# Kernel tuning notes

Hardware: AMD Instinct MI355X
Metric: run time of the kernel (lower is better)

The kernel has to match this reference:

```python
import jax, jax.numpy as jnp
import numpy as np

B, H, W = 2, 64, 64
D = 256  # in_channels
EPS = 1e-5


def conv2d(x, w, pad):
    # x: NCHW, w: OIHW
    return jax.lax.conv_general_dilated(
        x, w, window_strides=(1, 1), padding=[(pad, pad), (pad, pad)],
        dimension_numbers=("NCHW", "OIHW", "NCHW"))


def code_projection(X, codewords, scale):
    # X: [B, D, H, W]; codewords: [K, D]; scale: [D, K]
    b, d = X.shape[0], X.shape[1]
    x = X.reshape(b, d, -1).transpose(0, 2, 1)              # [B, N, D]
    # residual: [B, N, D, K] (large broadcast tensor, as in the original)
    residual = (x[:, :, :, None] - codewords.T[None, None]) * scale
    Q = jax.nn.softmax(-0.5 * jnp.sum(residual ** 2, axis=2), axis=-1)  # [B, N, K]
    Z_num = jnp.einsum("bnk,bndk->bdk", Q, residual)        # sum over N
    Z_ = Z_num / Q.sum(axis=1)[:, None, :]                  # [B, D, K]
    Z = Z_ / jnp.sqrt(jnp.sum(Z_ ** 2, axis=1, keepdims=True))  # L2 over D
    return Z, Q


def graph_conv(inp, weight, gamma, beta):
    # inp: [B, D, K]
    adj = jnp.einsum("bdk,bdl->bkl", inp, inp)              # input^T @ input
    support = jnp.einsum("ij,bjk->bik", weight, inp)        # weight @ input
    out = jnp.einsum("bdk,bkl->bdl", support, adj)          # support @ adj
    out = jax.nn.relu(out)
    # BatchNorm1d (training-mode batch stats over (B, K) per channel D)
    mean = out.mean(axis=(0, 2), keepdims=True)
    var = out.var(axis=(0, 2), keepdims=True)
    return gamma[None, :, None] * (out - mean) / jnp.sqrt(var + EPS) + beta[None, :, None]


def reproj(graph, Q, h, w):
    # graph: [B, D, K], Q: [B, N, K]
    x = jnp.einsum("bdk,bnk->bdn", graph, Q)
    return x.reshape(graph.shape[0], graph.shape[1], h, w)


def branch(c, conv_w, cw, sc, gcnw, g, bta, ext_w, h, w):
    z, q = code_projection(conv2d(c, conv_w, 1), cw, sc)
    z = graph_conv(z, gcnw, g, bta)
    return conv2d(reproj(z, q, h, w), ext_w, 0) + c


def setup_inputs() -> dict:
    key = jax.random.key(0)
    keys = iter(jax.random.split(key, 64))
    nk = lambda: next(keys)
    inp = {}
    inp["c3"] = jax.random.normal(nk(), (B, 512, H, W), jnp.float32)
    inp["c4"] = jax.random.normal(nk(), (B, 512, H, W), jnp.float32)
    inp["c5"] = jax.random.normal(nk(), (B, 512, H, W), jnp.float32)
    for name, K in [("32", 32), ("16", 16), ("8", 8)]:
        inp[f"conv{name}_w"] = jax.random.normal(nk(), (256, 512, 3, 3), jnp.float32) * 0.02
        std1 = 1.0 / np.sqrt(K * D)
        inp[f"cw{name}"] = jax.random.uniform(nk(), (K, D), jnp.float32, -std1, std1)
        inp[f"sc{name}"] = jax.random.uniform(nk(), (D, K), jnp.float32, -1.0, 0.0)
        stdv = 1.0 / np.sqrt(D)
        inp[f"gcnw{name}"] = jax.random.uniform(nk(), (D, D), jnp.float32, -stdv, stdv)
        inp[f"bng{name}"] = jax.random.uniform(nk(), (D,), jnp.float32, 0.5, 1.5)
        inp[f"bnb{name}"] = jax.random.normal(nk(), (D,), jnp.float32) * 0.1
        inp[f"ext{name}_w"] = jax.random.normal(nk(), (512, 256, 1, 1), jnp.float32) * 0.05
    inp["smooth_w"] = jax.random.normal(nk(), (512, 1536, 3, 3), jnp.float32) * 0.01
    inp["smg"] = jax.random.uniform(nk(), (512,), jnp.float32, 0.5, 1.5)
    inp["smb"] = jax.random.normal(nk(), (512,), jnp.float32) * 0.1
    return inp


def reference(c3, c4, c5,
              conv32_w, cw32, sc32, gcnw32, bng32, bnb32, ext32_w,
              conv16_w, cw16, sc16, gcnw16, bng16, bnb16, ext16_w,
              conv8_w, cw8, sc8, gcnw8, bng8, bnb8, ext8_w,
              smooth_w, smg, smb):
    h, w = c3.shape[2], c3.shape[3]
    x_32 = branch(c3, conv32_w, cw32, sc32, gcnw32, bng32, bnb32, ext32_w, h, w)
    x_16 = branch(c4, conv16_w, cw16, sc16, gcnw16, bng16, bnb16, ext16_w, h, w)
    x_8 = branch(c5, conv8_w, cw8, sc8, gcnw8, bng8, bnb8, ext8_w, h, w)
    out = jnp.concatenate([x_8, x_16, x_32], axis=1)        # [B, 1536, H, W]
    out = conv2d(out, smooth_w, 1)
    # BatchNorm2d (training-mode batch stats) + ReLU
    mean = out.mean(axis=(0, 2, 3), keepdims=True)
    var = out.var(axis=(0, 2, 3), keepdims=True)
    out = smg[None, :, None, None] * (out - mean) / jnp.sqrt(var + EPS) + smb[None, :, None, None]
    return jax.nn.relu(out)
```

## Files before the change

### kernel.cpp

```cpp
#include <hip/hip_runtime.h>
#include <hip/hip_bf16.h>
#include <math.h>

#define HWN 4096
#define DCH 256
#define EPSV 1e-5f

typedef unsigned short u16;
typedef __attribute__((ext_vector_type(8))) short short8b;
typedef __attribute__((ext_vector_type(4))) float fx4;
typedef __attribute__((ext_vector_type(8))) unsigned short u16x8;

static __device__ inline u16 f2bf(float f) {
  __hip_bfloat16 h = __float2bfloat16(f);
  return *reinterpret_cast<u16*>(&h);
}
static __device__ inline float bf2f(u16 u) {
  unsigned int v = ((unsigned int)u) << 16;
  return __uint_as_float(v);
}

__global__ __launch_bounds__(256) void t_chwc3_k(const float* __restrict__ i0p,
    const float* __restrict__ i1p, const float* __restrict__ i2p,
    u16* __restrict__ out) {
  __shared__ float tl[32][257];
  const int p0 = blockIdx.x * 256, cic = blockIdx.y;
  const int z = blockIdx.z;
  const int br = z >> 1, b = z & 1;
  const float* in = (br == 0) ? i0p : ((br == 1) ? i1p : i2p);
  const int t = threadIdx.x;
  const float* ip = in + ((size_t)(b * 512 + cic * 32)) * HWN + p0;
#pragma unroll
  for (int r = 0; r < 32; ++r) tl[r][t] = ip[(size_t)r * HWN + t];
  __syncthreads();
  u16* op = out + ((size_t)((z * 16 + cic)) * HWN + p0 + t) * 32;
#pragma unroll
  for (int g = 0; g < 4; ++g) {
    u16x8 o;
#pragma unroll
    for (int j = 0; j < 8; ++j) o[j] = f2bf(tl[g * 8 + j][t]);
    *reinterpret_cast<u16x8*>(op + g * 8) = o;
  }
}

template<int CIN, int COUT>
__global__ __launch_bounds__(256) void wpack_k(const float* __restrict__ w0,
    const float* __restrict__ w1, const float* __restrict__ w2,
    u16* __restrict__ wp) {
  constexpr int NCIC = CIN / 32, NCOG = COUT / 16;
  const int br = blockIdx.y;
  const float* w = (br == 0) ? w0 : ((br == 1) ? w1 : w2);
  u16* wpb = wp + (size_t)br * 9 * NCIC * NCOG * 512;
  const int cog = blockIdx.x % NCOG, cic = blockIdx.x / NCOG;
  __shared__ float ws_[16 * 32 * 9];
  const int t = threadIdx.x;
  const float* src = w + ((size_t)(cog * 16) * CIN + cic * 32) * 9;
  for (int i = t; i < 4608; i += 256) {
    int co = i / 288, r = i % 288;
    ws_[i] = src[(size_t)co * CIN * 9 + r];
  }
  __syncthreads();
  const size_t tapstride = (size_t)NCIC * NCOG * 512;
  const size_t base = ((size_t)cic * NCOG + cog) * 512;
#pragma unroll
  for (int tap = 0; tap < 9; ++tap) {
#pragma unroll
    for (int e0 = 0; e0 < 512; e0 += 256) {
      int e = e0 + t;
      int kg = e >> 7, m = (e >> 3) & 15, j = e & 7;
      wpb[tap * tapstride + base + e] = f2bf(ws_[m * 288 + (kg * 8 + j) * 9 + tap]);
    }
  }
}

template<int CIN, int COUT, int SPLIT, int COW, int WPE, bool BF16OUT>
__global__ __launch_bounds__(256, WPE) void convsp_k(
    const u16* __restrict__ xt, const u16* __restrict__ wp,
    void* __restrict__ outv) {
  constexpr int NCIC = CIN / 32;
  constexpr int NCO = COUT / COW;
  constexpr int NWT = COW / 16;
  constexpr int CICPS = NCIC / SPLIT;
  constexpr size_t OUTEL = (size_t)2 * COUT * HWN;
  const int br = blockIdx.y;
  xt += (size_t)br * 2 * NCIC * HWN * 32;
  wp += (size_t)br * 9 * NCIC * (COUT / 16) * 512;

  int g = blockIdx.x;
  const int cpx = (int)gridDim.x >> 3;
  g = (g & 7) * cpx + (g >> 3);
  const int s = g / (32 * NCO);
  const int rem = g % (32 * NCO);
  const int rt = rem / NCO;
  const int cob = (rem % NCO) * COW;

  const int wv = threadIdx.x >> 6, lane = threadIdx.x & 63;
  const int row = rt * 4 + wv;
  const int b = row >> 6, h = row & 63;
  const int m = lane & 15, kg = lane >> 4;

  fx4 acc[4][NWT];
#pragma unroll
  for (int i = 0; i < 4; ++i)
#pragma unroll
    for (int jn = 0; jn < NWT; ++jn) acc[i][jn] = (fx4){0.f, 0.f, 0.f, 0.f};

  const short8b zero8 = (short8b){0, 0, 0, 0, 0, 0, 0, 0};

#pragma unroll 1
  for (int cic = s * CICPS; cic < (s + 1) * CICPS; ++cic) {
    const u16* xbase = xt + ((size_t)(b * NCIC + cic)) * HWN * 32;
#pragma unroll
    for (int ty = 0; ty < 3; ++ty) {
      const int hh = h + ty - 1;
      if ((unsigned)hh < 64u) {
        const u16* rowp = xbase + (size_t)hh * 2048 + kg * 8;
#pragma unroll
        for (int tx = 0; tx < 3; ++tx) {
          short8b a[4];
#pragma unroll
          for (int mt = 0; mt < 4; ++mt) {
            int wi = mt * 16 + m + tx - 1;
            bool ok = ((unsigned)wi < 64u);
            int wc = ok ? wi : 0;
            short8b v = *reinterpret_cast<const short8b*>(rowp + wc * 32);
            a[mt] = ok ? v : zero8;
          }
          const int tap = ty * 3 + tx;
          const u16* wt = wp + (((size_t)tap * NCIC + cic) * (COUT / 16)
                                + (cob >> 4)) * 512 + lane * 8;
          short8b bb[NWT];
#pragma unroll
          for (int nt = 0; nt < NWT; ++nt)
            bb[nt] = *reinterpret_cast<const short8b*>(wt + nt * 512);
#pragma unroll
          for (int mt = 0; mt < 4; ++mt)
#pragma unroll
            for (int nt = 0; nt < NWT; ++nt)
              acc[mt][nt] = __builtin_amdgcn_mfma_f32_16x16x32_bf16(a[mt], bb[nt], acc[mt][nt], 0, 0, 0);
        }
      }
    }
  }

#pragma unroll
  for (int mt = 0; mt < 4; ++mt)
#pragma unroll
    for (int nt = 0; nt < NWT; ++nt) {
      int co = cob + nt * 16 + m;
      size_t idx = ((size_t)(b * COUT + co)) * HWN + h * 64 + mt * 16 + kg * 4;
      if (BF16OUT) {
        u16* op = (u16*)outv + (size_t)(br * SPLIT + s) * OUTEL + idx;
        ushort4 o;
        o.x = f2bf(acc[mt][nt][0]); o.y = f2bf(acc[mt][nt][1]);
        o.z = f2bf(acc[mt][nt][2]); o.w = f2bf(acc[mt][nt][3]);
        *reinterpret_cast<ushort4*>(op) = o;
      } else {
        float* op = (float*)outv + (size_t)(br * SPLIT + s) * OUTEL + idx;
        *reinterpret_cast<fx4*>(op) = acc[mt][nt];
      }
    }
}

__global__ __launch_bounds__(256) void breduce_k(const u16* __restrict__ slab,
    float* __restrict__ X) {
  const int br = blockIdx.x >> 10;
  const size_t el = (size_t)2 * DCH * HWN;
  const u16* sb = slab + (size_t)br * 2 * el;
  float* Xb = X + (size_t)br * el;
  const size_t i0 = ((size_t)(blockIdx.x & 1023) * 256 + threadIdx.x) * 8;
  u16x8 s0 = *reinterpret_cast<const u16x8*>(sb + i0);
  u16x8 s1 = *reinterpret_cast<const u16x8*>(sb + el + i0);
  fx4 o0, o1;
#pragma unroll
  for (int j = 0; j < 4; ++j) o0[j] = bf2f(s0[j]) + bf2f(s1[j]);
#pragma unroll
  for (int j = 0; j < 4; ++j) o1[j] = bf2f(s0[4 + j]) + bf2f(s1[4 + j]);
  *reinterpret_cast<fx4*>(Xb + i0) = o0;
  *reinterpret_cast<fx4*>(Xb + i0 + 4) = o1;
}

__global__ __launch_bounds__(256) void sreduce_bn_k(const u16* __restrict__ slab,
    float* __restrict__ dout, float* __restrict__ pstat) {
  const int o = blockIdx.x, b = blockIdx.y;
  const size_t el = (size_t)2 * 512 * HWN;
  const size_t base = ((size_t)(b * 512 + o)) * HWN;
  const int t = threadIdx.x;
  float s = 0.f, ss = 0.f;
#pragma unroll
  for (int i0 = t * 8; i0 < HWN; i0 += 256 * 8) {
    u16x8 v0 = *reinterpret_cast<const u16x8*>(slab + base + i0);
    u16x8 v1 = *reinterpret_cast<const u16x8*>(slab + el + base + i0);
    u16x8 v2 = *reinterpret_cast<const u16x8*>(slab + 2 * el + base + i0);
    u16x8 v3 = *reinterpret_cast<const u16x8*>(slab + 3 * el + base + i0);
    fx4 y0, y1;
#pragma unroll
    for (int j = 0; j < 4; ++j) {
      float y = (bf2f(v0[j]) + bf2f(v1[j])) + (bf2f(v2[j]) + bf2f(v3[j]));
      y0[j] = y; s += y; ss = fmaf(y, y, ss);
    }
#pragma unroll
    for (int j = 0; j < 4; ++j) {
      float y = (bf2f(v0[4 + j]) + bf2f(v1[4 + j])) + (bf2f(v2[4 + j]) + bf2f(v3[4 + j]));
      y1[j] = y; s += y; ss = fmaf(y, y, ss);
    }
    *reinterpret_cast<fx4*>(dout + base + i0) = y0;
    *reinterpret_cast<fx4*>(dout + base + i0 + 4) = y1;
  }
  __shared__ float rs[4], rss[4];
  for (int off = 32; off; off >>= 1) { s += __shfl_down(s, off); ss += __shfl_down(ss, off); }
  int lane = t & 63, wid = t >> 6;
  if (lane == 0) { rs[wid] = s; rss[wid] = ss; }
  __syncthreads();
  if (t == 0) {
    pstat[(b * 512 + o) * 2]     = rs[0] + rs[1] + rs[2] + rs[3];
    pstat[(b * 512 + o) * 2 + 1] = rss[0] + rss[1] + rss[2] + rss[3];
  }
}

__global__ __launch_bounds__(512) void bnfin_k(const float* __restrict__ pstat,
    float* __restrict__ stat) {
  const int o = threadIdx.x;
  float S  = pstat[o * 2] + pstat[(512 + o) * 2];
  float SS = pstat[o * 2 + 1] + pstat[(512 + o) * 2 + 1];
  float mean = S / (2 * HWN);
  float var  = SS / (2 * HWN) - mean * mean;
  stat[o] = mean;
  stat[512 + o] = 1.f / sqrtf(var + EPSV);
}

__global__ __launch_bounds__(256) void prep3_k(
    const float* __restrict__ sc0, const float* __restrict__ sc1, const float* __restrict__ sc2,
    const float* __restrict__ cw0, const float* __restrict__ cw1, const float* __restrict__ cw2,
    float2* __restrict__ AB, float* __restrict__ Ck) {
  const int br = blockIdx.y;
  const int K = 8 << br;
  const int k = blockIdx.x;
  if (k >= K) return;
  const float* sc = (br == 0) ? sc0 : ((br == 1) ? sc1 : sc2);
  const float* cw = (br == 0) ? cw0 : ((br == 1) ? cw1 : cw2);
  float2* ABb = AB + 2048 * ((1 << br) - 1);
  float* Ckb = Ck + 8 * ((1 << br) - 1);
  const int d = threadIdx.x;
  float s = sc[d * K + k];
  float a = s * s;
  float c = cw[k * DCH + d];
  ABb[d * K + k] = make_float2(a, c * a);
  float tt = c * s;
  tt = tt * tt;
  __shared__ float red[4];
  for (int off = 32; off; off >>= 1) tt += __shfl_down(tt, off);
  int lane = threadIdx.x & 63, wid = threadIdx.x >> 6;
  if (lane == 0) red[wid] = tt;
  __syncthreads();
  if (threadIdx.x == 0) Ckb[k] = red[0] + red[1] + red[2] + red[3];
}

template<int K>
static __device__ void score_body(int b, float* sm, const float* __restrict__ X,
    const float2* __restrict__ AB, const float* __restrict__ Ck,
    float* __restrict__ Qt, float* __restrict__ Qsp) {
  const int lane = threadIdx.x & 63;
  const int g = threadIdx.x >> 6;
  const int n = blockIdx.x * 64 + lane;
  const float* xp = X + ((size_t)b * DCH) * HWN + n;
  float s_[K];
#pragma unroll
  for (int k = 0; k < K; ++k) s_[k] = 0.f;
  for (int d = g * 64; d < g * 64 + 64; ++d) {
    float xv = xp[(size_t)d * HWN];
    float x2 = xv * xv;
    float xm = -2.f * xv;
    const float2* abp = AB + d * K;
#pragma unroll
    for (int k = 0; k < K; ++k) {
      float2 ab = abp[k];
      s_[k] = fmaf(x2, ab.x, s_[k]);
      s_[k] = fmaf(xm, ab.y, s_[k]);
    }
  }
  float* smr = sm + (g * 64 + lane) * (K + 1);
#pragma unroll
  for (int k = 0; k < K; ++k) smr[k] = s_[k];
  __syncthreads();
  if (g == 0) {
    const float* r0 = sm + lane * (K + 1);
    const float* r1 = sm + (64 + lane) * (K + 1);
    const float* r2 = sm + (128 + lane) * (K + 1);
    const float* r3 = sm + (192 + lane) * (K + 1);
    float mx = -1e30f;
#pragma unroll
    for (int k = 0; k < K; ++k) {
      float v = (r0[k] + r1[k]) + (r2[k] + r3[k]);
      s_[k] = -0.5f * (v + Ck[k]);
      mx = fmaxf(mx, s_[k]);
    }
    float sum = 0.f;
#pragma unroll
    for (int k = 0; k < K; ++k) { float e = expf(s_[k] - mx); s_[k] = e; sum += e; }
    float inv = 1.f / sum;
#pragma unroll
    for (int k = 0; k < K; ++k) {
      float v = s_[k] * inv;
      Qt[((size_t)(b * K + k)) * HWN + n] = v;
      for (int off = 32; off; off >>= 1) v += __shfl_down(v, off);
      if (lane == 0) Qsp[((size_t)(b * K + k)) * 64 + blockIdx.x] = v;
    }
  }
}

__global__ __launch_bounds__(256) void score3_k(const float* __restrict__ X3,
    const float2* __restrict__ AB3, const float* __restrict__ Ck3,
    float* __restrict__ Qt3, float* __restrict__ Qsp3) {
  __shared__ float sm[4 * 64 * 33];
  const int z = blockIdx.y, br = z >> 1, b = z & 1;
  const size_t XEL = (size_t)2 * DCH * HWN;
  if (br == 0)
    score_body<8>(b, sm, X3, AB3, Ck3, Qt3, Qsp3);
  else if (br == 1)
    score_body<16>(b, sm, X3 + XEL, AB3 + 2048, Ck3 + 8, Qt3 + 65536, Qsp3 + 1024);
  else
    score_body<32>(b, sm, X3 + 2 * XEL, AB3 + 6144, Ck3 + 24, Qt3 + 196608, Qsp3 + 3072);
}

template<int K>
static __device__ void mmulp_body(int b, float* xs, float* pw,
    const float* __restrict__ X, const float* __restrict__ Qt,
    float* __restrict__ Mp) {
  const int d = blockIdx.x, nch = blockIdx.y;
  const int t = threadIdx.x;
  const float* xp = X + ((size_t)(b * DCH + d)) * HWN + nch * 512;
  xs[t] = xp[t]; xs[t + 256] = xp[t + 256];
  __syncthreads();
  const int lane = t & 63, wid = t >> 6;
#pragma unroll
  for (int k = 0; k < K; ++k) {
    const float* qp = Qt + ((size_t)(b * K + k)) * HWN + nch * 512;
    float s = fmaf(xs[t], qp[t], xs[t + 256] * qp[t + 256]);
    for (int off = 32; off; off >>= 1) s += __shfl_down(s, off);
    if (lane == 0) pw[wid * 33 + k] = s;
  }
  __syncthreads();
  if (t < K)
    Mp[(((size_t)(b * DCH + d)) * K + t) * 8 + nch] =
        (pw[t] + pw[33 + t]) + (pw[66 + t] + pw[99 + t]);
}

__global__ __launch_bounds__(256) void mmulp3_k(const float* __restrict__ X3,
    const float* __restrict__ Qt3, float* __restrict__ Mp3) {
  __shared__ float xs[512];
  __shared__ float pw[4 * 33];
  const int z = blockIdx.z, br = z >> 1, b = z & 1;
  const size_t XEL = (size_t)2 * DCH * HWN;
  if (br == 0)
    mmulp_body<8>(b, xs, pw, X3, Qt3, Mp3);
  else if (br == 1)
    mmulp_body<16>(b, xs, pw, X3 + XEL, Qt3 + 65536, Mp3 + 32768);
  else
    mmulp_body<32>(b, xs, pw, X3 + 2 * XEL, Qt3 + 196608, Mp3 + 98304);
}

template<int K>
static __device__ void fuse1_body(int b, float* buf, const float* __restrict__ Mp,
    const float* __restrict__ Qsp, const float* __restrict__ sc,
    const float* __restrict__ cw, const float* __restrict__ Wm,
    float* __restrict__ Graw) {
  float* zl = buf;
  float* adj = zl + DCH * K;
  float* rn = adj + K * K;
  float* qsl = rn + K;
  const int t = threadIdx.x;
  if (t < K) {
    const float* qp = Qsp + ((size_t)(b * K + t)) * 64;
    float s = 0.f;
    for (int i = 0; i < 64; ++i) s += qp[i];
    qsl[t] = s;
  }
  __syncthreads();
#pragma unroll
  for (int k = 0; k < K; ++k) {
    const float* mp = Mp + (((size_t)(b * DCH + t)) * K + k) * 8;
    fx4 p0 = *reinterpret_cast<const fx4*>(mp);
    fx4 p1 = *reinterpret_cast<const fx4*>(mp + 4);
    float mm = ((p0[0] + p0[1]) + (p0[2] + p0[3])) + ((p1[0] + p1[1]) + (p1[2] + p1[3]));
    float qs = qsl[k];
    zl[t * K + k] = sc[t * K + k] * (mm - cw[k * DCH + t] * qs) / qs;
  }
  __syncthreads();
  if (t < K) {
    float s = 0.f;
    for (int i = 0; i < DCH; ++i) { float v = zl[i * K + t]; s = fmaf(v, v, s); }
    rn[t] = 1.f / sqrtf(s);
  }
  __syncthreads();
#pragma unroll
  for (int k = 0; k < K; ++k) zl[t * K + k] *= rn[k];
  __syncthreads();
  for (int p = t; p < K * K; p += 256) {
    int k = p / K, l = p % K;
    float s = 0.f;
    for (int i = 0; i < DCH; ++i) s = fmaf(zl[i * K + k], zl[i * K + l], s);
    adj[p] = s;
  }
  __syncthreads();
  float sup[K];
#pragma unroll
  for (int k = 0; k < K; ++k) sup[k] = 0.f;
  const float* wr = Wm + (size_t)t * DCH;
  for (int jj = 0; jj < DCH; ++jj) {
    float wv = wr[jj];
#pragma unroll
    for (int k = 0; k < K; ++k) sup[k] = fmaf(wv, zl[jj * K + k], sup[k]);
  }
#pragma unroll
  for (int l = 0; l < K; ++l) {
    float s = 0.f;
#pragma unroll
    for (int k = 0; k < K; ++k) s = fmaf(sup[k], adj[k * K + l], s);
    Graw[((size_t)(b * DCH + t)) * K + l] = fmaxf(s, 0.f);
  }
}

__global__ __launch_bounds__(256) void fuse13_k(const float* __restrict__ Mp3,
    const float* __restrict__ Qsp3,
    const float* __restrict__ sc0, const float* __restrict__ sc1, const float* __restrict__ sc2,
    const float* __restrict__ cw0, const float* __restrict__ cw1, const float* __restrict__ cw2,
    const float* __restrict__ wm0, const float* __restrict__ wm1, const float* __restrict__ wm2,
    float* __restrict__ Graw3) {
  __shared__ float buf[DCH * 32 + 32 * 32 + 64];
  const int z = blockIdx.x, br = z >> 1, b = z & 1;
  if (br == 0)
    fuse1_body<8>(b, buf, Mp3, Qsp3, sc0, cw0, wm0, Graw3);
  else if (br == 1)
    fuse1_body<16>(b, buf, Mp3 + 32768, Qsp3 + 1024, sc1, cw1, wm1, Graw3 + 4096);
  else
    fuse1_body<32>(b, buf, Mp3 + 98304, Qsp3 + 3072, sc2, cw2, wm2, Graw3 + 12288);
}

template<int K>
static __device__ void fuse2_body(int b, int ob, float* gl,
    const float* __restrict__ Graw, const float* __restrict__ gamma,
    const float* __restrict__ beta, const float* __restrict__ E,
    float* __restrict__ EG) {
  const int t = threadIdx.x;
  {
    const int d = t;
    float s = 0.f, ss = 0.f;
#pragma unroll
    for (int b2 = 0; b2 < 2; ++b2)
#pragma unroll
      for (int l = 0; l < K; ++l) {
        float v = Graw[((size_t)(b2 * DCH + d)) * K + l];
        s += v; ss = fmaf(v, v, ss);
      }
    const float invn = 1.f / (2 * K);
    float mean = s * invn;
    float var  = ss * invn - mean * mean;
    float giv  = gamma[d] / sqrtf(var + EPSV);
    float be   = beta[d];
#pragma unroll
    for (int l = 0; l < K; ++l) {
      float v = Graw[((size_t)(b * DCH + d)) * K + l];
      gl[d * K + l] = fmaf(v - mean, giv, be);
    }
  }
  __syncthreads();
  const int o = ob * 256 + t;
  float a[K];
#pragma unroll
  for (int k = 0; k < K; ++k) a[k] = 0.f;
  const fx4* e4 = reinterpret_cast<const fx4*>(E + (size_t)o * DCH);
  for (int d4 = 0; d4 < 64; ++d4) {
    fx4 v = e4[d4];
#pragma unroll
    for (int j = 0; j < 4; ++j) {
      float vv = v[j];
#pragma unroll
      for (int k = 0; k < K; ++k)
        a[k] = fmaf(vv, gl[(d4 * 4 + j) * K + k], a[k]);
    }
  }
#pragma unroll
  for (int k = 0; k < K; ++k)
    EG[((size_t)(b * 512 + o)) * K + k] = a[k];
}

__global__ __launch_bounds__(256) void fuse23_k(const float* __restrict__ Graw3,
    const float* __restrict__ g0, const float* __restrict__ g1, const float* __restrict__ g2,
    const float* __restrict__ b0, const float* __restrict__ b1, const float* __restrict__ b2,
    const float* __restrict__ e0, const float* __restrict__ e1, const float* __restrict__ e2,
    float* __restrict__ EG3) {
  __shared__ float gl[DCH * 32];
  const int b = blockIdx.x, ob = blockIdx.y, br = blockIdx.z;
  if (br == 0)
    fuse2_body<8>(b, ob, gl, Graw3, g0, b0, e0, EG3);
  else if (br == 1)
    fuse2_body<16>(b, ob, gl, Graw3 + 4096, g1, b1, e1, EG3 + 8192);
  else
    fuse2_body<32>(b, ob, gl, Graw3 + 12288, g2, b2, e2, EG3 + 24576);
}

template<int K>
static __device__ void yout_body(int b, u16* egl, const float* __restrict__ EG,
    const float* __restrict__ Qt, const float* __restrict__ cres,
    u16* __restrict__ cat, int coff) {
  const int cg = blockIdx.y;
  const int t = threadIdx.x;
  const int lane = t & 63, sub = t >> 6;
  const int n = blockIdx.x * 64 + lane;
  for (int i = t; i < K * 128; i += 256) {
    int k = i >> 7, co = i & 127;
    egl[i] = f2bf(EG[((size_t)(b * 512 + cg * 128 + co)) * K + k]);
  }
  float q[K];
#pragma unroll
  for (int k = 0; k < K; ++k) q[k] = Qt[((size_t)(b * K + k)) * HWN + n];
  __syncthreads();
  const float* crow = cres + (size_t)b * 512 * HWN + n;
#pragma unroll
  for (int it = 0; it < 4; ++it) {
    int co = sub * 32 + it * 8;
    int gco = cg * 128 + co;
    float y[8];
#pragma unroll
    for (int jj = 0; jj < 8; ++jj) y[jj] = crow[(size_t)(gco + jj) * HWN];
#pragma unroll
    for (int k = 0; k < K; ++k) {
      u16x8 eg = *reinterpret_cast<const u16x8*>(&egl[k * 128 + co]);
#pragma unroll
      for (int jj = 0; jj < 8; ++jj) y[jj] = fmaf(bf2f(eg[jj]), q[k], y[jj]);
    }
    u16x8 o;
#pragma unroll
    for (int jj = 0; jj < 8; ++jj) o[jj] = f2bf(y[jj]);
    int ch = coff + gco;
    *reinterpret_cast<u16x8*>(cat +
        (((size_t)(b * 48 + (ch >> 5)) * HWN + n) * 32 + (ch & 31))) = o;
  }
}

__global__ __launch_bounds__(256) void yout3_k(const float* __restrict__ EG3,
    const float* __restrict__ Qt3, const float* __restrict__ c5,
    const float* __restrict__ c4, const float* __restrict__ c3,
    u16* __restrict__ cat) {
  __shared__ u16 egl[32 * 128];
  const int z = blockIdx.z, br = z >> 1, b = z & 1;
  if (br == 0)
    yout_body<8>(b, egl, EG3, Qt3, c5, cat, 0);
  else if (br == 1)
    yout_body<16>(b, egl, EG3 + 8192, Qt3 + 65536, c4, cat, 512);
  else
    yout_body<32>(b, egl, EG3 + 24576, Qt3 + 196608, c3, cat, 1024);
}

__global__ __launch_bounds__(256) void bnrelu_k(float* __restrict__ out,
    const float* __restrict__ stat, const float* __restrict__ g,
    const float* __restrict__ bb) {
  int idx = blockIdx.x * 256 + threadIdx.x;
  int o = (idx >> 12) & 511;
  float v = out[idx];
  float r = fmaf((v - stat[o]) * stat[512 + o], g[o], bb[o]);
  out[idx] = fmaxf(r, 0.f);
}

extern "C" void kernel_launch(void* const* d_in, const int* in_sizes, int n_in,
                              void* d_out, int out_size, void* d_ws, size_t ws_size,
                              hipStream_t stream) {
  const float* c3 = (const float*)d_in[0];
  const float* c4 = (const float*)d_in[1];
  const float* c5 = (const float*)d_in[2];
  const float* smooth_w = (const float*)d_in[24];
  const float* smg = (const float*)d_in[25];
  const float* smb = (const float*)d_in[26];
  float* dout = (float*)d_out;

  char* wsb = (char*)d_ws;
  u16* Xt3 = (u16*)wsb;
  u16* cat = (u16*)wsb;
  u16* Wb  = (u16*)(wsb + 25165824);
  float* stat  = (float*)(wsb + 39321600);
  float* pstat = (float*)(wsb + 39325696);
  float* pool  = (float*)(wsb + 39346176);
  char* C = wsb + 43540480;
  u16* bslab   = (u16*)C;
  float* X3    = (float*)(C + 25165824);
  u16* sslab   = (u16*)C;

  float* Qt3  = pool;
  float* Qsp3 = pool + 458752;
  float* Mp3  = pool + 465920;
  float* Graw3 = pool + 723968;
  float* EG3  = pool + 752640;
  float2* AB3 = (float2*)(pool + 809984);
  float* Ck3  = pool + 838656;

  t_chwc3_k<<<dim3(16, 16, 6), 256, 0, stream>>>(c5, c4, c3, Xt3);
  wpack_k<512, 256><<<dim3(256, 3), 256, 0, stream>>>(
      (const float*)d_in[17], (const float*)d_in[10], (const float*)d_in[3], Wb);
  convsp_k<512, 256, 2, 64, 4, true><<<dim3(256, 3), 256, 0, stream>>>(Xt3, Wb, bslab);
  breduce_k<<<3072, 256, 0, stream>>>(bslab, X3);

  prep3_k<<<dim3(32, 3), 256, 0, stream>>>(
      (const float*)d_in[19], (const float*)d_in[12], (const float*)d_in[5],
      (const float*)d_in[18], (const float*)d_in[11], (const float*)d_in[4],
      AB3, Ck3);
  score3_k<<<dim3(64, 6), 256, 0, stream>>>(X3, AB3, Ck3, Qt3, Qsp3);
  mmulp3_k<<<dim3(256, 8, 6), 256, 0, stream>>>(X3, Qt3, Mp3);
  fuse13_k<<<6, 256, 0, stream>>>(Mp3, Qsp3,
      (const float*)d_in[19], (const float*)d_in[12], (const float*)d_in[5],
      (const float*)d_in[18], (const float*)d_in[11], (const float*)d_in[4],
      (const float*)d_in[20], (const float*)d_in[13], (const float*)d_in[6],
      Graw3);
  fuse23_k<<<dim3(2, 2, 3), 256, 0, stream>>>(Graw3,
      (const float*)d_in[21], (const float*)d_in[14], (const float*)d_in[7],
      (const float*)d_in[22], (const float*)d_in[15], (const float*)d_in[8],
      (const float*)d_in[23], (const float*)d_in[16], (const float*)d_in[9],
      EG3);
  yout3_k<<<dim3(64, 4, 6), 256, 0, stream>>>(EG3, Qt3, c5, c4, c3, cat);

  wpack_k<1536, 512><<<dim3(1536, 1), 256, 0, stream>>>(smooth_w, smooth_w, smooth_w, Wb);
  convsp_k<1536, 512, 4, 128, 2, true><<<dim3(512, 1), 256, 0, stream>>>(cat, Wb, sslab);
  sreduce_bn_k<<<dim3(512, 2), 256, 0, stream>>>(sslab, dout, pstat);
  bnfin_k<<<1, 512, 0, stream>>>(pstat, stat);
  bnrelu_k<<<16384, 256, 0, stream>>>(dout, stat, smg, smb);
}
```

Measured before the change: 488.6 us.

## Stage conv weights in double-buffered LDS and fuse split-K reduce into scoring

The implicit-GEMM conv kernel now cooperatively loads each tap-row's weight tiles into a double-buffered shared-memory array, prefetching the next stage into registers while MFMAs run on the current one. Previously every wave loaded the weights straight from global memory. Separately, the standalone bf16 split-K reduction kernel is removed, and the scoring kernel sums the two partial slabs itself, writing X on the fly. This cuts global weight traffic and one kernel launch with its extra pass over the data. In exchange it adds shared-memory use, a barrier per stage, and lower occupancy (the first conv's launch bound drops from 4 to 3 waves per EU).

```diff
diff --git a/kernel.cpp b/kernel.cpp
--- a/kernel.cpp
+++ b/kernel.cpp
@@ -74,14 +74,20 @@
 }
 
 template<int CIN, int COUT, int SPLIT, int COW, int WPE, bool BF16OUT>
-__global__ __launch_bounds__(256, WPE) void convsp_k(
+__global__ __launch_bounds__(256, WPE) void convlds_k(
     const u16* __restrict__ xt, const u16* __restrict__ wp,
     void* __restrict__ outv) {
   constexpr int NCIC = CIN / 32;
   constexpr int NCO = COUT / COW;
   constexpr int NWT = COW / 16;
   constexpr int CICPS = NCIC / SPLIT;
+  constexpr int NST = CICPS * 3;
+  constexpr int TAPB = COW * 32;
+  constexpr int WSH = TAPB / 4;
+  constexpr int RNDS = WSH / 512;
   constexpr size_t OUTEL = (size_t)2 * COUT * HWN;
+  __shared__ u16 bl[2][3 * TAPB];
+
   const int br = blockIdx.y;
   xt += (size_t)br * 2 * NCIC * HWN * 32;
   wp += (size_t)br * 9 * NCIC * (COUT / 16) * 512;
@@ -98,6 +104,7 @@
   const int row = rt * 4 + wv;
   const int b = row >> 6, h = row & 63;
   const int m = lane & 15, kg = lane >> 4;
+  const int cic0 = s * CICPS;
 
   fx4 acc[4][NWT];
 #pragma unroll
@@ -106,41 +113,74 @@
     for (int jn = 0; jn < NWT; ++jn) acc[i][jn] = (fx4){0.f, 0.f, 0.f, 0.f};
 
   const short8b zero8 = (short8b){0, 0, 0, 0, 0, 0, 0, 0};
+  const int lds_lane = wv * WSH + lane * 8;
+
+  {
+    const int cic = cic0, ty = 0;
+#pragma unroll
+    for (int t3 = 0; t3 < 3; ++t3) {
+      const int tap = ty * 3 + t3;
+      const u16* srcb = wp + (((size_t)tap * NCIC + cic) * (COUT / 16) + (cob >> 4)) * 512;
+#pragma unroll
+      for (int r = 0; r < RNDS; ++r) {
+        u16x8 v = *reinterpret_cast<const u16x8*>(srcb + lds_lane + r * 512);
+        *reinterpret_cast<u16x8*>(&bl[0][t3 * TAPB + lds_lane + r * 512]) = v;
+      }
+    }
+  }
+  __syncthreads();
 
 #pragma unroll 1
-  for (int cic = s * CICPS; cic < (s + 1) * CICPS; ++cic) {
-    const u16* xbase = xt + ((size_t)(b * NCIC + cic)) * HWN * 32;
-#pragma unroll
-    for (int ty = 0; ty < 3; ++ty) {
-      const int hh = h + ty - 1;
-      if ((unsigned)hh < 64u) {
-        const u16* rowp = xbase + (size_t)hh * 2048 + kg * 8;
-#pragma unroll
-        for (int tx = 0; tx < 3; ++tx) {
-          short8b a[4];
-#pragma unroll
-          for (int mt = 0; mt < 4; ++mt) {
-            int wi = mt * 16 + m + tx - 1;
-            bool ok = ((unsigned)wi < 64u);
-            int wc = ok ? wi : 0;
-            short8b v = *reinterpret_cast<const short8b*>(rowp + wc * 32);
-            a[mt] = ok ? v : zero8;
-          }
-          const int tap = ty * 3 + tx;
-          const u16* wt = wp + (((size_t)tap * NCIC + cic) * (COUT / 16)
-                                + (cob >> 4)) * 512 + lane * 8;
-          short8b bb[NWT];
+  for (int st = 0; st < NST; ++st) {
+    const int cur = st & 1;
+    u16x8 stg[3][RNDS];
+    const bool hasnext = (st + 1 < NST);
+    if (hasnext) {
+      const int cicn = cic0 + (st + 1) / 3, tyn = (st + 1) % 3;
+#pragma unroll
+      for (int t3 = 0; t3 < 3; ++t3) {
+        const int tap = tyn * 3 + t3;
+        const u16* srcb = wp + (((size_t)tap * NCIC + cicn) * (COUT / 16) + (cob >> 4)) * 512;
+#pragma unroll
+        for (int r = 0; r < RNDS; ++r)
+          stg[t3][r] = *reinterpret_cast<const u16x8*>(srcb + lds_lane + r * 512);
+      }
+    }
+    const int cic = cic0 + st / 3, ty = st % 3;
+    const int hh = h + ty - 1;
+    if ((unsigned)hh < 64u) {
+      const u16* rowp = xt + ((size_t)(b * NCIC + cic)) * HWN * 32
+                        + (size_t)hh * 2048 + kg * 8;
+#pragma unroll
+      for (int tx = 0; tx < 3; ++tx) {
+        short8b a[4];
+#pragma unroll
+        for (int mt = 0; mt < 4; ++mt) {
+          int wi = mt * 16 + m + tx - 1;
+          bool ok = ((unsigned)wi < 64u);
+          int wc = ok ? wi : 0;
+          short8b v = *reinterpret_cast<const short8b*>(rowp + wc * 32);
+          a[mt] = ok ? v : zero8;
+        }
+        short8b bb[NWT];
+#pragma unroll
+        for (int nt = 0; nt < NWT; ++nt)
+          bb[nt] = *reinterpret_cast<const short8b*>(&bl[cur][tx * TAPB + nt * 512 + lane * 8]);
+#pragma unroll
+        for (int mt = 0; mt < 4; ++mt)
 #pragma unroll
           for (int nt = 0; nt < NWT; ++nt)
-            bb[nt] = *reinterpret_cast<const short8b*>(wt + nt * 512);
-#pragma unroll
-          for (int mt = 0; mt < 4; ++mt)
-#pragma unroll
-            for (int nt = 0; nt < NWT; ++nt)
-              acc[mt][nt] = __builtin_amdgcn_mfma_f32_16x16x32_bf16(a[mt], bb[nt], acc[mt][nt], 0, 0, 0);
-        }
+            acc[mt][nt] = __builtin_amdgcn_mfma_f32_16x16x32_bf16(a[mt], bb[nt], acc[mt][nt], 0, 0, 0);
       }
     }
+    if (hasnext) {
+#pragma unroll
+      for (int t3 = 0; t3 < 3; ++t3)
+#pragma unroll
+        for (int r = 0; r < RNDS; ++r)
+          *reinterpret_cast<u16x8*>(&bl[cur ^ 1][t3 * TAPB + lds_lane + r * 512]) = stg[t3][r];
+    }
+    __syncthreads();
   }
 
 #pragma unroll
@@ -160,24 +200,6 @@
         *reinterpret_cast<fx4*>(op) = acc[mt][nt];
       }
     }
-}
-
-__global__ __launch_bounds__(256) void breduce_k(const u16* __restrict__ slab,
-    float* __restrict__ X) {
-  const int br = blockIdx.x >> 10;
-  const size_t el = (size_t)2 * DCH * HWN;
-  const u16* sb = slab + (size_t)br * 2 * el;
-  float* Xb = X + (size_t)br * el;
-  const size_t i0 = ((size_t)(blockIdx.x & 1023) * 256 + threadIdx.x) * 8;
-  u16x8 s0 = *reinterpret_cast<const u16x8*>(sb + i0);
-  u16x8 s1 = *reinterpret_cast<const u16x8*>(sb + el + i0);
-  fx4 o0, o1;
-#pragma unroll
-  for (int j = 0; j < 4; ++j) o0[j] = bf2f(s0[j]) + bf2f(s1[j]);
-#pragma unroll
-  for (int j = 0; j < 4; ++j) o1[j] = bf2f(s0[4 + j]) + bf2f(s1[4 + j]);
-  *reinterpret_cast<fx4*>(Xb + i0) = o0;
-  *reinterpret_cast<fx4*>(Xb + i0 + 4) = o1;
 }
 
 __global__ __launch_bounds__(256) void sreduce_bn_k(const u16* __restrict__ slab,
@@ -257,18 +279,22 @@
 }
 
 template<int K>
-static __device__ void score_body(int b, float* sm, const float* __restrict__ X,
+static __device__ void score_body(int b, float* sm,
+    const u16* __restrict__ s0p, const u16* __restrict__ s1p,
+    float* __restrict__ Xout,
     const float2* __restrict__ AB, const float* __restrict__ Ck,
     float* __restrict__ Qt, float* __restrict__ Qsp) {
   const int lane = threadIdx.x & 63;
   const int g = threadIdx.x >> 6;
   const int n = blockIdx.x * 64 + lane;
-  const float* xp = X + ((size_t)b * DCH) * HWN + n;
+  const size_t bbase = ((size_t)b * DCH) * HWN + n;
   float s_[K];
 #pragma unroll
   for (int k = 0; k < K; ++k) s_[k] = 0.f;
   for (int d = g * 64; d < g * 64 + 64; ++d) {
-    float xv = xp[(size_t)d * HWN];
+    const size_t ofs = bbase + (size_t)d * HWN;
+    float xv = bf2f(s0p[ofs]) + bf2f(s1p[ofs]);
+    Xout[ofs] = xv;
     float x2 = xv * xv;
     float xm = -2.f * xv;
     const float2* abp = AB + d * K;
@@ -309,18 +335,21 @@
   }
 }
 
-__global__ __launch_bounds__(256) void score3_k(const float* __restrict__ X3,
+__global__ __launch_bounds__(256) void score3_k(const u16* __restrict__ bslab,
+    float* __restrict__ X3,
     const float2* __restrict__ AB3, const float* __restrict__ Ck3,
     float* __restrict__ Qt3, float* __restrict__ Qsp3) {
   __shared__ float sm[4 * 64 * 33];
   const int z = blockIdx.y, br = z >> 1, b = z & 1;
   const size_t XEL = (size_t)2 * DCH * HWN;
+  const u16* s0 = bslab + (size_t)br * 2 * XEL;
+  const u16* s1 = s0 + XEL;
   if (br == 0)
-    score_body<8>(b, sm, X3, AB3, Ck3, Qt3, Qsp3);
+    score_body<8>(b, sm, s0, s1, X3, AB3, Ck3, Qt3, Qsp3);
   else if (br == 1)
-    score_body<16>(b, sm, X3 + XEL, AB3 + 2048, Ck3 + 8, Qt3 + 65536, Qsp3 + 1024);
+    score_body<16>(b, sm, s0, s1, X3 + XEL, AB3 + 2048, Ck3 + 8, Qt3 + 65536, Qsp3 + 1024);
   else
-    score_body<32>(b, sm, X3 + 2 * XEL, AB3 + 6144, Ck3 + 24, Qt3 + 196608, Qsp3 + 3072);
+    score_body<32>(b, sm, s0, s1, X3 + 2 * XEL, AB3 + 6144, Ck3 + 24, Qt3 + 196608, Qsp3 + 3072);
 }
 
 template<int K>
@@ -597,14 +626,13 @@
   t_chwc3_k<<<dim3(16, 16, 6), 256, 0, stream>>>(c5, c4, c3, Xt3);
   wpack_k<512, 256><<<dim3(256, 3), 256, 0, stream>>>(
       (const float*)d_in[17], (const float*)d_in[10], (const float*)d_in[3], Wb);
-  convsp_k<512, 256, 2, 64, 4, true><<<dim3(256, 3), 256, 0, stream>>>(Xt3, Wb, bslab);
-  breduce_k<<<3072, 256, 0, stream>>>(bslab, X3);
+  convlds_k<512, 256, 2, 64, 3, true><<<dim3(256, 3), 256, 0, stream>>>(Xt3, Wb, bslab);
 
   prep3_k<<<dim3(32, 3), 256, 0, stream>>>(
       (const float*)d_in[19], (const float*)d_in[12], (const float*)d_in[5],
       (const float*)d_in[18], (const float*)d_in[11], (const float*)d_in[4],
       AB3, Ck3);
-  score3_k<<<dim3(64, 6), 256, 0, stream>>>(X3, AB3, Ck3, Qt3, Qsp3);
+  score3_k<<<dim3(64, 6), 256, 0, stream>>>(bslab, X3, AB3, Ck3, Qt3, Qsp3);
   mmulp3_k<<<dim3(256, 8, 6), 256, 0, stream>>>(X3, Qt3, Mp3);
   fuse13_k<<<6, 256, 0, stream>>>(Mp3, Qsp3,
       (const float*)d_in[19], (const float*)d_in[12], (const float*)d_in[5],
@@ -619,7 +647,7 @@
   yout3_k<<<dim3(64, 4, 6), 256, 0, stream>>>(EG3, Qt3, c5, c4, c3, cat);
 
   wpack_k<1536, 512><<<dim3(1536, 1), 256, 0, stream>>>(smooth_w, smooth_w, smooth_w, Wb);
-  convsp_k<1536, 512, 4, 128, 2, true><<<dim3(512, 1), 256, 0, stream>>>(cat, Wb, sslab);
+  convlds_k<1536, 512, 4, 128, 2, true><<<dim3(512, 1), 256, 0, stream>>>(cat, Wb, sslab);
   sreduce_bn_k<<<dim3(512, 2), 256, 0, stream>>>(sslab, dout, pstat);
   bnfin_k<<<1, 512, 0, stream>>>(pstat, stat);
   bnrelu_k<<<16384, 256, 0, stream>>>(dout, stat, smg, smb);
```

After: 466.8 us. 1.05x faster.
